# Kernel tuning notes

Hardware: AMD Instinct MI355X
Metric: run time of the kernel (lower is better)

The kernel has to match this reference:

```python
import jax, jax.numpy as jnp
import numpy as np

B, N, L = 1, 2048, 256
DIM_X, DIM_Y, H = 3072, 1536, 24
HD = DIM_X // H  # 128
EPS_MOD = 1e-6   # modulated_rmsnorm eps
EPS_QK = 1e-5    # RMSNorm (q/k norm) eps
NEG = -1e30


def _rms(v, w, eps):
    return v * jax.lax.rsqrt(jnp.mean(v * v, axis=-1, keepdims=True) + eps) * w


def _rope(t, cos, sin):
    # t: (B, N, H, HD); cos/sin: (N, H, HD//2); interleaved even/odd rotation
    te, to = t[..., 0::2], t[..., 1::2]
    c, s = cos[None], sin[None]
    out = jnp.stack([te * c - to * s, te * s + to * c], axis=-1)
    return out.reshape(t.shape)


def _forward(x, y, scale_x, scale_y, rope_cos, rope_sin,
             W_qkv_x, b_qkv_x, W_qkv_y, b_qkv_y,
             w_qnorm_x, w_knorm_x, w_qnorm_y, w_knorm_y,
             W_proj_x, b_proj_x, W_proj_y, b_proj_y, seqlens_y):
    # modulated RMSNorm on x, then fused qkv projection
    xm = x * jax.lax.rsqrt(jnp.mean(x * x, axis=-1, keepdims=True) + EPS_MOD) * (1.0 + scale_x[:, None, :])
    qkv_x = (xm @ W_qkv_x.T + b_qkv_x).reshape(B, N, 3, H, HD)
    q_x, k_x, v_x = qkv_x[:, :, 0], qkv_x[:, :, 1], qkv_x[:, :, 2]
    q_x = _rope(_rms(q_x, w_qnorm_x, EPS_QK), rope_cos, rope_sin)
    k_x = _rope(_rms(k_x, w_knorm_x, EPS_QK), rope_cos, rope_sin)

    ym = y * jax.lax.rsqrt(jnp.mean(y * y, axis=-1, keepdims=True) + EPS_MOD) * (1.0 + scale_y[:, None, :])
    qkv_y = (ym @ W_qkv_y.T + b_qkv_y).reshape(B, L, 3, H, HD)
    q_y, k_y, v_y = qkv_y[:, :, 0], qkv_y[:, :, 1], qkv_y[:, :, 2]
    q_y = _rms(q_y, w_qnorm_y, EPS_QK)
    k_y = _rms(k_y, w_knorm_y, EPS_QK)

    # unify_streams: concat visual + text tokens; flash_attn_varlen over valid
    # tokens == masked dense attention (all x tokens valid, y valid up to seqlens_y)
    q = jnp.concatenate([q_x, q_y], axis=1)  # (B, N+L, H, HD)
    k = jnp.concatenate([k_x, k_y], axis=1)
    v = jnp.concatenate([v_x, v_y], axis=1)
    valid_y = jnp.arange(L)[None, :] < seqlens_y[:, None]          # (B, L)
    valid = jnp.concatenate([jnp.ones((B, N), bool), valid_y], 1)  # (B, N+L)

    scale = HD ** -0.5
    logits = jnp.einsum('bqhd,bkhd->bhqk', q, k) * scale
    logits = jnp.where(valid[:, None, None, :], logits, NEG)
    attn = jax.nn.softmax(logits, axis=-1)
    out = jnp.einsum('bhqk,bkhd->bqhd', attn, v)
    # pad_and_split_xy: invalid positions are zeros (scatter into zero buffer)
    out = jnp.where(valid[:, :, None, None], out, 0.0).reshape(B, N + L, DIM_X)

    x_out = out[:, :N] @ W_proj_x.T + b_proj_x
    y_out = out[:, N:] @ W_proj_y.T + b_proj_y
    return x_out, y_out


def setup_inputs() -> dict:
    key = jax.random.key(0)
    ks = jax.random.split(key, 16)
    f32 = jnp.float32
    theta = jax.random.uniform(ks[4], (N, H, HD // 2), f32, 0.0, 2 * np.pi)
    return {
        'x': jax.random.normal(ks[0], (B, N, DIM_X), f32),
        'y': jax.random.normal(ks[1], (B, L, DIM_Y), f32),
        'scale_x': 0.1 * jax.random.normal(ks[2], (B, DIM_X), f32),
        'scale_y': 0.1 * jax.random.normal(ks[3], (B, DIM_Y), f32),
        'rope_cos': jnp.cos(theta),
        'rope_sin': jnp.sin(theta),
        'seqlens_y': jax.random.randint(ks[5], (B,), 1, L + 1, jnp.int32),
        'W_qkv_x': 0.02 * jax.random.normal(ks[6], (3 * DIM_X, DIM_X), f32),
        'b_qkv_x': jnp.zeros((3 * DIM_X,), f32),
        'W_qkv_y': 0.02 * jax.random.normal(ks[7], (3 * DIM_X, DIM_Y), f32),
        'b_qkv_y': jnp.zeros((3 * DIM_X,), f32),
        'w_qnorm_x': jnp.ones((HD,), f32),
        'w_knorm_x': jnp.ones((HD,), f32),
        'w_qnorm_y': jnp.ones((HD,), f32),
        'w_knorm_y': jnp.ones((HD,), f32),
        'W_proj_x': 0.02 * jax.random.normal(ks[8], (DIM_X, DIM_X), f32),
        'b_proj_x': jnp.zeros((DIM_X,), f32),
        'W_proj_y': 0.02 * jax.random.normal(ks[9], (DIM_Y, DIM_X), f32),
        'b_proj_y': jnp.zeros((DIM_Y,), f32),
    }


def reference(x, y, scale_x, scale_y, rope_cos, rope_sin, seqlens_y,
              W_qkv_x, b_qkv_x, W_qkv_y, b_qkv_y,
              w_qnorm_x, w_knorm_x, w_qnorm_y, w_knorm_y,
              W_proj_x, b_proj_x, W_proj_y, b_proj_y):
    return _forward(x, y, scale_x, scale_y, rope_cos, rope_sin,
                    W_qkv_x, b_qkv_x, W_qkv_y, b_qkv_y,
                    w_qnorm_x, w_knorm_x, w_qnorm_y, w_knorm_y,
                    W_proj_x, b_proj_x, W_proj_y, b_proj_y, seqlens_y)
```

## Files before the change

### kernel.cpp

```cpp
#include <hip/hip_runtime.h>
#include <stdint.h>

#define DEV __device__ __forceinline__

typedef __attribute__((ext_vector_type(8))) short bf16x8;
typedef __attribute__((ext_vector_type(4))) float f32x4;
typedef __attribute__((ext_vector_type(16))) float f32x16;
typedef __attribute__((ext_vector_type(4))) unsigned u32x4;

#define NTOT 2304

DEV unsigned short f2bf(float f) {
  union { float f; unsigned u; } c; c.f = f;
  return (unsigned short)((c.u + 0x7FFFu + ((c.u >> 16) & 1u)) >> 16);
}
DEV unsigned pack2(float lo, float hi) {
  return ((unsigned)f2bf(hi) << 16) | (unsigned)f2bf(lo);
}
DEV unsigned cvtpk(float lo, float hi) {
  unsigned r;
  asm("v_cvt_pk_bf16_f32 %0, %1, %2" : "=v"(r) : "v"(lo), "v"(hi));
  return r;
}
DEV float bf2f(short x) {
  union { unsigned u; float f; } c; c.u = ((unsigned)(unsigned short)x) << 16; return c.f;
}
DEV void gload_lds16(const void* g, void* l) {
  __builtin_amdgcn_global_load_lds(
      (const __attribute__((address_space(1))) unsigned int*)g,
      (__attribute__((address_space(3))) unsigned int*)l, 16, 0, 0);
}
DEV void pl32swap(unsigned& a, unsigned& b) {
  asm volatile("v_permlane32_swap_b32 %0, %1" : "+v"(a), "+v"(b));
}

__global__ __launch_bounds__(256) void k_modnorm(const float* __restrict__ X,
                                                 const float* __restrict__ scale_x,
                                                 short* __restrict__ outx,
                                                 const float* __restrict__ Y,
                                                 const float* __restrict__ scale_y,
                                                 short* __restrict__ outy) {
  int row = blockIdx.x;
  const float* x;
  const float* scale;
  short* o;
  int D;
  if (row < 2048) {
    x = X + (size_t)row * 3072; scale = scale_x; o = outx + (size_t)row * 3072; D = 3072;
  } else {
    row -= 2048;
    x = Y + (size_t)row * 1536; scale = scale_y; o = outy + (size_t)row * 1536; D = 1536;
  }
  float ss = 0.f;
  for (int v = threadIdx.x * 4; v < D; v += 1024) {
    float4 a = *(const float4*)(x + v);
    ss += a.x * a.x + a.y * a.y + a.z * a.z + a.w * a.w;
  }
#pragma unroll
  for (int m = 1; m < 64; m <<= 1) ss += __shfl_xor(ss, m);
  __shared__ float red[4];
  if ((threadIdx.x & 63) == 0) red[threadIdx.x >> 6] = ss;
  __syncthreads();
  float tot = red[0] + red[1] + red[2] + red[3];
  float r = rsqrtf(tot / (float)D + 1e-6f);
  for (int v = threadIdx.x * 4; v < D; v += 1024) {
    float4 a = *(const float4*)(x + v);
    float4 s = *(const float4*)(scale + v);
    uint2 pk;
    pk.x = pack2(a.x * r * (1.f + s.x), a.y * r * (1.f + s.y));
    pk.y = pack2(a.z * r * (1.f + s.z), a.w * r * (1.f + s.w));
    *(uint2*)(o + v) = pk;
  }
}

__global__ __launch_bounds__(256) void k_cvt4(const float* __restrict__ s0, short* __restrict__ d0, int n0,
                                              const float* __restrict__ s1, short* __restrict__ d1, int n1,
                                              const float* __restrict__ s2, short* __restrict__ d2, int n2,
                                              const float* __restrict__ s3, short* __restrict__ d3, int n3) {
  int total = n0 + n1 + n2 + n3;
  int stride = gridDim.x * blockDim.x;
  for (int i = blockIdx.x * blockDim.x + threadIdx.x; i < total; i += stride) {
    const float* s; short* d; int j = i;
    if (j < n0) { s = s0; d = d0; }
    else {
      j -= n0;
      if (j < n1) { s = s1; d = d1; }
      else {
        j -= n1;
        if (j < n2) { s = s2; d = d2; }
        else { j -= n2; s = s3; d = d3; }
      }
    }
    float4 a = *(const float4*)(s + (size_t)j * 4);
    uint2 pk;
    pk.x = pack2(a.x, a.y);
    pk.y = pack2(a.z, a.w);
    *(uint2*)(d + (size_t)j * 4) = pk;
  }
}

__global__ __launch_bounds__(256) void k_gemm(const short* __restrict__ A,
                                              const short* __restrict__ B,
                                              const float* __restrict__ bias,
                                              float* __restrict__ C, int M, int N, int K) {
  __shared__ __align__(16) char As[16384];
  __shared__ __align__(16) char Bs[16384];
  const int tid = threadIdx.x;
  const int brow = blockIdx.y * 128, bcol = blockIdx.x * 128;
  const int w = tid >> 6, l = tid & 63;
  const int wr = (w >> 1) * 64, wc = (w & 1) * 64;
  const int lr = l & 15, lg = l >> 4;
  f32x4 acc[4][4];
#pragma unroll
  for (int m = 0; m < 4; ++m)
#pragma unroll
    for (int n = 0; n < 4; ++n) acc[m][n] = (f32x4){0.f, 0.f, 0.f, 0.f};
  for (int k0 = 0; k0 < K; k0 += 64) {
#pragma unroll
    for (int it = 0; it < 4; ++it) {
      int o = it * 4096 + tid * 16;
      int row = o >> 7;
      int gs = ((o >> 4) & 7) ^ (row & 7);
      gload_lds16(A + (size_t)(brow + row) * K + k0 + gs * 8, As + o);
      gload_lds16(B + (size_t)(bcol + row) * K + k0 + gs * 8, Bs + o);
    }
    __syncthreads();
#pragma unroll
    for (int ks = 0; ks < 2; ++ks) {
      bf16x8 af[4], bfr[4];
#pragma unroll
      for (int m = 0; m < 4; ++m) {
        int ra = wr + m * 16 + lr;
        af[m] = *(const bf16x8*)(As + ra * 128 + (((ks * 4 + lg) ^ (ra & 7)) << 4));
        int rb = wc + m * 16 + lr;
        bfr[m] = *(const bf16x8*)(Bs + rb * 128 + (((ks * 4 + lg) ^ (rb & 7)) << 4));
      }
#pragma unroll
      for (int m = 0; m < 4; ++m)
#pragma unroll
        for (int n = 0; n < 4; ++n)
          acc[m][n] = __builtin_amdgcn_mfma_f32_16x16x32_bf16(bfr[n], af[m], acc[m][n], 0, 0, 0);
    }
    __syncthreads();
  }
#pragma unroll
  for (int m = 0; m < 4; ++m) {
    int row = brow + wr + m * 16 + lr;
#pragma unroll
    for (int n = 0; n < 4; ++n) {
      int col = bcol + wc + n * 16 + lg * 4;
      float4 bv = *(const float4*)(bias + col);
      float4 o;
      o.x = acc[m][n][0] + bv.x;
      o.y = acc[m][n][1] + bv.y;
      o.z = acc[m][n][2] + bv.z;
      o.w = acc[m][n][3] + bv.w;
      *(float4*)(C + (size_t)row * N + col) = o;
    }
  }
}

__global__ __launch_bounds__(256) void k_gemm_qkv(const short* __restrict__ A,
                                                  const short* __restrict__ B,
                                                  const float* __restrict__ bias,
                                                  short* __restrict__ Qb, short* __restrict__ Kb,
                                                  short* __restrict__ Vb,
                                                  int K, int col0, int base_n) {
  __shared__ __align__(16) char As[16384];
  __shared__ __align__(16) char Bs[16384];
  const int tid = threadIdx.x;
  const int brow = blockIdx.y * 128, bcol = blockIdx.x * 128;
  const int w = tid >> 6, l = tid & 63;
  const int wr = (w >> 1) * 64, wc = (w & 1) * 64;
  const int lr = l & 15, lg = l >> 4;
  f32x4 acc[4][4];
#pragma unroll
  for (int m = 0; m < 4; ++m)
#pragma unroll
    for (int n = 0; n < 4; ++n) acc[m][n] = (f32x4){0.f, 0.f, 0.f, 0.f};
  for (int k0 = 0; k0 < K; k0 += 64) {
#pragma unroll
    for (int it = 0; it < 4; ++it) {
      int o = it * 4096 + tid * 16;
      int row = o >> 7;
      int gs = ((o >> 4) & 7) ^ (row & 7);
      gload_lds16(A + (size_t)(brow + row) * K + k0 + gs * 8, As + o);
      gload_lds16(B + (size_t)(bcol + row) * K + k0 + gs * 8, Bs + o);
    }
    __syncthreads();
#pragma unroll
    for (int ks = 0; ks < 2; ++ks) {
      bf16x8 af[4], bfr[4];
#pragma unroll
      for (int m = 0; m < 4; ++m) {
        int ra = wr + m * 16 + lr;
        af[m] = *(const bf16x8*)(As + ra * 128 + (((ks * 4 + lg) ^ (ra & 7)) << 4));
        int rb = wc + m * 16 + lr;
        bfr[m] = *(const bf16x8*)(Bs + rb * 128 + (((ks * 4 + lg) ^ (rb & 7)) << 4));
      }
#pragma unroll
      for (int m = 0; m < 4; ++m)
#pragma unroll
        for (int n = 0; n < 4; ++n)
          acc[m][n] = __builtin_amdgcn_mfma_f32_16x16x32_bf16(bfr[n], af[m], acc[m][n], 0, 0, 0);
    }
    __syncthreads();
  }
#pragma unroll
  for (int m = 0; m < 4; ++m) {
    int row = brow + wr + m * 16 + lr;
#pragma unroll
    for (int n = 0; n < 4; ++n) {
      int colg = col0 + bcol + wc + n * 16 + lg * 4;
      float4 bv = *(const float4*)(bias + colg);
      int ty = colg / 3072;
      int rem = colg - ty * 3072;
      int h = rem >> 7, d = rem & 127;
      short* dst = (ty == 0) ? Qb : ((ty == 1) ? Kb : Vb);
      uint2 pk;
      pk.x = pack2(acc[m][n][0] + bv.x, acc[m][n][1] + bv.y);
      pk.y = pack2(acc[m][n][2] + bv.z, acc[m][n][3] + bv.w);
      *(uint2*)(dst + ((size_t)(h * NTOT + base_n + row)) * 128 + d) = pk;
    }
  }
}

__global__ __launch_bounds__(512, 2) void k_g256(const short* __restrict__ A,
                                                 const short* __restrict__ B,
                                                 const float* __restrict__ bias,
                                                 short* __restrict__ Qb, short* __restrict__ Kb,
                                                 short* __restrict__ Vb, int K) {
  __shared__ __align__(16) char lds[131072];
  const int tid = threadIdx.x;
  const int w = tid >> 6, l = tid & 63;
  const int lr = l & 15, lg = l >> 4;
  const int wm = w >> 2, wn = w & 3;
  const int brow = blockIdx.y * 256, bcol = blockIdx.x * 256;
  const int nt = K >> 6;

  auto issue = [&](int g) {
    if (g >= 4 * nt) return;
    int tt = g >> 2, hh = g & 3;
    char* base = lds + (tt & 1) * 65536;
    if (hh < 2) {
#pragma unroll
      for (int j = 0; j < 2; ++j) {
        int ch = hh * 1024 + j * 512 + tid;
        int row = ch >> 3, c = ch & 7;
        gload_lds16(A + (size_t)(brow + row) * K + tt * 64 + ((c ^ (row & 7)) << 3),
                    base + ch * 16);
      }
    } else {
      int hb = hh - 2;
#pragma unroll
      for (int j = 0; j < 2; ++j) {
        int ch = hb * 1024 + j * 512 + tid;
        int row = ch >> 3, c = ch & 7;
        gload_lds16(B + (size_t)(bcol + row) * K + tt * 64 + ((c ^ (row & 7)) << 3),
                    base + 32768 + ch * 16);
      }
    }
  };

  f32x4 acc[8][4];
#pragma unroll
  for (int m = 0; m < 8; ++m)
#pragma unroll
    for (int n = 0; n < 4; ++n) acc[m][n] = (f32x4){0.f, 0.f, 0.f, 0.f};

#pragma unroll
  for (int g = 0; g < 6; ++g) issue(g);
  asm volatile("s_waitcnt vmcnt(4)" ::: "memory");
  __builtin_amdgcn_s_barrier();

  bf16x8 af[8][2], bf[4][2];
  for (int t = 0; t < nt; ++t) {
    const char* bb = lds + (t & 1) * 65536;
    const int g0 = 4 * t + 6;
#pragma unroll
    for (int m = 0; m < 4; ++m) {
      int r = wm * 128 + m * 16 + lr;
#pragma unroll
      for (int ks = 0; ks < 2; ++ks)
        af[m][ks] = *(const bf16x8*)(bb + r * 128 + (((ks * 4 + lg) ^ (r & 7)) << 4));
    }
#pragma unroll
    for (int n = 0; n < 2; ++n) {
      int r = wn * 64 + n * 16 + lr;
#pragma unroll
      for (int ks = 0; ks < 2; ++ks)
        bf[n][ks] = *(const bf16x8*)(bb + 32768 + r * 128 + (((ks * 4 + lg) ^ (r & 7)) << 4));
    }
    issue(g0);
    __builtin_amdgcn_s_barrier();
    __builtin_amdgcn_s_setprio(1);
#pragma unroll
    for (int m = 0; m < 4; ++m)
#pragma unroll
      for (int n = 0; n < 2; ++n)
#pragma unroll
        for (int ks = 0; ks < 2; ++ks)
          acc[m][n] = __builtin_amdgcn_mfma_f32_16x16x32_bf16(bf[n][ks], af[m][ks], acc[m][n], 0, 0, 0);
    __builtin_amdgcn_s_setprio(0);
    __builtin_amdgcn_sched_barrier(0);
    __builtin_amdgcn_s_barrier();
#pragma unroll
    for (int n = 2; n < 4; ++n) {
      int r = wn * 64 + n * 16 + lr;
#pragma unroll
      for (int ks = 0; ks < 2; ++ks)
        bf[n][ks] = *(const bf16x8*)(bb + 32768 + r * 128 + (((ks * 4 + lg) ^ (r & 7)) << 4));
    }
    issue(g0 + 1);
    __builtin_amdgcn_s_barrier();
    __builtin_amdgcn_s_setprio(1);
#pragma unroll
    for (int m = 0; m < 4; ++m)
#pragma unroll
      for (int n = 2; n < 4; ++n)
#pragma unroll
        for (int ks = 0; ks < 2; ++ks)
          acc[m][n] = __builtin_amdgcn_mfma_f32_16x16x32_bf16(bf[n][ks], af[m][ks], acc[m][n], 0, 0, 0);
    __builtin_amdgcn_s_setprio(0);
    __builtin_amdgcn_sched_barrier(0);
    __builtin_amdgcn_s_barrier();
#pragma unroll
    for (int m = 4; m < 8; ++m) {
      int r = wm * 128 + m * 16 + lr;
#pragma unroll
      for (int ks = 0; ks < 2; ++ks)
        af[m][ks] = *(const bf16x8*)(bb + r * 128 + (((ks * 4 + lg) ^ (r & 7)) << 4));
    }
    __builtin_amdgcn_s_barrier();
    __builtin_amdgcn_s_setprio(1);
#pragma unroll
    for (int m = 4; m < 8; ++m)
#pragma unroll
      for (int n = 2; n < 4; ++n)
#pragma unroll
        for (int ks = 0; ks < 2; ++ks)
          acc[m][n] = __builtin_amdgcn_mfma_f32_16x16x32_bf16(bf[n][ks], af[m][ks], acc[m][n], 0, 0, 0);
    __builtin_amdgcn_s_setprio(0);
    __builtin_amdgcn_sched_barrier(0);
    __builtin_amdgcn_s_barrier();
    issue(g0 + 2);
    issue(g0 + 3);
    __builtin_amdgcn_s_barrier();
    __builtin_amdgcn_s_setprio(1);
#pragma unroll
    for (int m = 4; m < 8; ++m)
#pragma unroll
      for (int n = 0; n < 2; ++n)
#pragma unroll
        for (int ks = 0; ks < 2; ++ks)
          acc[m][n] = __builtin_amdgcn_mfma_f32_16x16x32_bf16(bf[n][ks], af[m][ks], acc[m][n], 0, 0, 0);
    __builtin_amdgcn_s_setprio(0);
    __builtin_amdgcn_sched_barrier(0);
    if (t + 2 < nt)
      asm volatile("s_waitcnt vmcnt(4)" ::: "memory");
    else
      asm volatile("s_waitcnt vmcnt(0)" ::: "memory");
    __builtin_amdgcn_s_barrier();
  }

#pragma unroll
  for (int m = 0; m < 8; ++m) {
    int row = brow + wm * 128 + m * 16 + lr;
#pragma unroll
    for (int n = 0; n < 4; ++n) {
      int colg = bcol + wn * 64 + n * 16 + lg * 4;
      float4 bv = *(const float4*)(bias + colg);
      int ty = colg / 3072;
      int rem = colg - ty * 3072;
      int h = rem >> 7, d = rem & 127;
      short* dst = (ty == 0) ? Qb : ((ty == 1) ? Kb : Vb);
      uint2 pk;
      pk.x = pack2(acc[m][n][0] + bv.x, acc[m][n][1] + bv.y);
      pk.y = pack2(acc[m][n][2] + bv.z, acc[m][n][3] + bv.w);
      *(uint2*)(dst + ((size_t)(h * NTOT + row)) * 128 + d) = pk;
    }
  }
}

__global__ __launch_bounds__(256) void k_post2(short* __restrict__ Qb, short* __restrict__ Kb,
                                               const float* __restrict__ wqx,
                                               const float* __restrict__ wkx,
                                               const float* __restrict__ wqy,
                                               const float* __restrict__ wky,
                                               const float* __restrict__ cosb,
                                               const float* __restrict__ sinb) {
  int idx = blockIdx.x * 4 + (threadIdx.x >> 6);
  int l = threadIdx.x & 63;
  const float* wq;
  const float* wk;
  int n, h, base_n;
  bool rope;
  if (idx < 49152) {
    n = idx / 24; h = idx - n * 24; base_n = 0; wq = wqx; wk = wkx; rope = true;
  } else {
    int j = idx - 49152;
    n = j / 24; h = j - n * 24; base_n = 2048; wq = wqy; wk = wky; rope = false;
  }
  size_t off = ((size_t)h * NTOT + base_n + n) * 128 + 2 * l;
  unsigned qu = *(unsigned*)(Qb + off);
  unsigned ku = *(unsigned*)(Kb + off);
  float qx = bf2f((short)(qu & 0xFFFF)), qy = bf2f((short)(qu >> 16));
  float kx = bf2f((short)(ku & 0xFFFF)), ky = bf2f((short)(ku >> 16));
  float sq = qx * qx + qy * qy;
  float sk = kx * kx + ky * ky;
#pragma unroll
  for (int m = 1; m < 64; m <<= 1) {
    sq += __shfl_xor(sq, m);
    sk += __shfl_xor(sk, m);
  }
  float rq = rsqrtf(sq * (1.f / 128.f) + 1e-5f);
  float rk = rsqrtf(sk * (1.f / 128.f) + 1e-5f);
  float2 wqv = *(const float2*)(wq + 2 * l);
  float2 wkv = *(const float2*)(wk + 2 * l);
  qx = qx * rq * wqv.x; qy = qy * rq * wqv.y;
  kx = kx * rk * wkv.x; ky = ky * rk * wkv.y;
  if (rope) {
    float c = cosb[(size_t)idx * 64 + l];
    float s = sinb[(size_t)idx * 64 + l];
    float t;
    t = qx * c - qy * s; qy = qx * s + qy * c; qx = t;
    t = kx * c - ky * s; ky = kx * s + ky * c; kx = t;
  }
  *(unsigned*)(Qb + off) = pack2(qx, qy);
  *(unsigned*)(Kb + off) = pack2(kx, ky);
}

__global__ __launch_bounds__(256) void k_transpose(const short* __restrict__ V,
                                                   short* __restrict__ VT) {
  __shared__ __align__(16) short tile[64][72];
  int h = blockIdx.z;
  int n0 = blockIdx.x * 64, d0 = blockIdx.y * 64;
  int tid = threadIdx.x;
#pragma unroll
  for (int it = 0; it < 2; ++it) {
    int nl = it * 32 + (tid >> 3);
    int dl = (tid & 7) * 8;
    *(bf16x8*)&tile[nl][dl] = *(const bf16x8*)(V + ((size_t)h * NTOT + n0 + nl) * 128 + d0 + dl);
  }
  __syncthreads();
#pragma unroll
  for (int it = 0; it < 2; ++it) {
    int dl = it * 32 + (tid >> 3);
    int nl = (tid & 7) * 8;
    bf16x8 o;
#pragma unroll
    for (int j = 0; j < 8; ++j) o[j] = tile[nl + j][dl];
    *(bf16x8*)(VT + ((size_t)h * 128 + d0 + dl) * NTOT + n0 + nl) = o;
  }
}

__global__ __launch_bounds__(256, 2) void k_attn32(const short* __restrict__ Qb,
                                                   const short* __restrict__ Kb,
                                                   const short* __restrict__ VT,
                                                   const int* __restrict__ seqlens,
                                                   short* __restrict__ Ob) {
  __shared__ __align__(16) char lds[65536];
  const int tid = threadIdx.x;
  const int w = tid >> 6, l = tid & 63;
  const int l31 = l & 31, hi = l >> 5;
  int orig = blockIdx.x;
  int wg = (orig & 7) * 54 + (orig >> 3);
  int h = wg / 18, qb = wg - h * 18;
  const int q0 = qb * 128;
  const size_t hK = (size_t)h * NTOT * 128;
  const size_t hV = (size_t)h * 128 * NTOT;
  const int kvlim = 2048 + seqlens[0];
  const int nt = (kvlim + 63) >> 6;

  const float qs = 0.08838834764831845f * 1.44269504088896340f;
  bf16x8 qf[8];
  {
    const short* qrow = Qb + hK + (size_t)(q0 + w * 32 + l31) * 128;
#pragma unroll
    for (int s = 0; s < 8; ++s) {
      bf16x8 r = *(const bf16x8*)(qrow + s * 16 + hi * 8);
      union { unsigned u[4]; bf16x8 b; } cv;
#pragma unroll
      for (int d = 0; d < 4; ++d)
        cv.u[d] = cvtpk(bf2f(r[2 * d]) * qs, bf2f(r[2 * d + 1]) * qs);
      qf[s] = cv.b;
    }
  }

  f32x16 acc[4];
#pragma unroll
  for (int d0 = 0; d0 < 4; ++d0)
#pragma unroll
    for (int r = 0; r < 16; ++r) acc[d0][r] = 0.f;
  float mrun = -1e30f, lsum = 0.f;

  auto stage = [&](int t, int buf) {
    int kv0 = t * 64;
    char* bK = lds + buf * 32768;
    char* bV = bK + 16384;
#pragma unroll
    for (int it = 0; it < 4; ++it) {
      int o = it * 4096 + tid * 16;
      int rk = o >> 8, sk = (o >> 4) & 15;
      int mk = (rk & 7) ^ ((rk >> 3) & 3);
      gload_lds16(Kb + hK + (size_t)(kv0 + rk) * 128 + ((sk ^ mk) << 3), bK + o);
      int rv = o >> 7, sv = (o >> 4) & 7;
      gload_lds16(VT + hV + (size_t)rv * NTOT + kv0 + ((sv ^ (rv & 7)) << 3), bV + o);
    }
  };

  stage(0, 0);
  asm volatile("s_waitcnt vmcnt(0)");
  __syncthreads();

  int cur = 0;
  for (int t = 0; t < nt; ++t) {
    if (t + 1 < nt) stage(t + 1, cur ^ 1);
    const char* bK = lds + cur * 32768;
    const char* bV = bK + 16384;
    f32x16 st[2];
#pragma unroll
    for (int hf = 0; hf < 2; ++hf)
#pragma unroll
      for (int r = 0; r < 16; ++r) st[hf][r] = 0.f;
#pragma unroll
    for (int hf = 0; hf < 2; ++hf) {
      int row = hf * 32 + l31;
      int mk = (row & 7) ^ ((row >> 3) & 3);
#pragma unroll
      for (int s = 0; s < 8; ++s) {
        bf16x8 kf = *(const bf16x8*)(bK + row * 256 + (((s * 2 + hi) ^ mk) << 4));
        st[hf] = __builtin_amdgcn_mfma_f32_32x32x16_bf16(kf, qf[s], st[hf], 0, 0, 0);
      }
    }
    if (t == nt - 1) {
      int kv0 = t * 64;
#pragma unroll
      for (int hf = 0; hf < 2; ++hf)
#pragma unroll
        for (int r = 0; r < 16; ++r) {
          int kv = kv0 + hf * 32 + (r & 3) + 8 * (r >> 2) + 4 * hi;
          if (kv >= kvlim) st[hf][r] = -1e30f;
        }
    }
    float tm[8];
#pragma unroll
    for (int i = 0; i < 8; ++i)
      tm[i] = fmaxf(fmaxf(st[0][2 * i], st[0][2 * i + 1]),
                    fmaxf(st[1][2 * i], st[1][2 * i + 1]));
    float tmax = fmaxf(fmaxf(fmaxf(tm[0], tm[1]), fmaxf(tm[2], tm[3])),
                       fmaxf(fmaxf(tm[4], tm[5]), fmaxf(tm[6], tm[7])));
    tmax = fmaxf(tmax, __shfl_xor(tmax, 32));
    if (!__all(tmax - mrun <= 11.54f)) {
      float mnew = fmaxf(mrun, tmax);
      float corr = __builtin_amdgcn_exp2f(mrun - mnew);
      mrun = mnew;
      lsum *= corr;
#pragma unroll
      for (int d0 = 0; d0 < 4; ++d0)
#pragma unroll
        for (int r = 0; r < 16; ++r) acc[d0][r] *= corr;
    }
    float ts = 0.f;
#pragma unroll
    for (int hf = 0; hf < 2; ++hf)
#pragma unroll
      for (int r = 0; r < 16; ++r) {
        float p = __builtin_amdgcn_exp2f(st[hf][r] - mrun);
        st[hf][r] = p;
        ts += p;
      }
    ts += __shfl_xor(ts, 32);
    lsum += ts;
    bf16x8 pa[4];
#pragma unroll
    for (int hf = 0; hf < 2; ++hf) {
      unsigned x0 = cvtpk(st[hf][0], st[hf][1]);
      unsigned y0 = cvtpk(st[hf][4], st[hf][5]);
      pl32swap(x0, y0);
      unsigned z0 = cvtpk(st[hf][2], st[hf][3]);
      unsigned w0 = cvtpk(st[hf][6], st[hf][7]);
      pl32swap(z0, w0);
      { union { u32x4 u; bf16x8 b; } cv; cv.u = (u32x4){x0, z0, y0, w0}; pa[hf * 2 + 0] = cv.b; }
      unsigned x1 = cvtpk(st[hf][8], st[hf][9]);
      unsigned y1 = cvtpk(st[hf][12], st[hf][13]);
      pl32swap(x1, y1);
      unsigned z1 = cvtpk(st[hf][10], st[hf][11]);
      unsigned w1 = cvtpk(st[hf][14], st[hf][15]);
      pl32swap(z1, w1);
      { union { u32x4 u; bf16x8 b; } cv; cv.u = (u32x4){x1, z1, y1, w1}; pa[hf * 2 + 1] = cv.b; }
    }
#pragma unroll
    for (int d0 = 0; d0 < 4; ++d0) {
      int row = d0 * 32 + l31;
      int rx = row & 7;
#pragma unroll
      for (int s4 = 0; s4 < 4; ++s4) {
        bf16x8 va = *(const bf16x8*)(bV + row * 128 + (((s4 * 2 + hi) ^ rx) << 4));
        acc[d0] = __builtin_amdgcn_mfma_f32_32x32x16_bf16(va, pa[s4], acc[d0], 0, 0, 0);
      }
    }
    asm volatile("s_waitcnt vmcnt(0)");
    __syncthreads();
    cur ^= 1;
  }

  {
    char* ob = lds;
    int qloc = w * 32 + l31;
    int qg = q0 + qloc;
    float inv = (qg < kvlim) ? 1.f / lsum : 0.f;
#pragma unroll
    for (int d0 = 0; d0 < 4; ++d0)
#pragma unroll
      for (int g = 0; g < 4; ++g) {
        int dbase = d0 * 32 + 8 * g + 4 * hi;
        uint2 pk;
        pk.x = cvtpk(acc[d0][4 * g + 0] * inv, acc[d0][4 * g + 1] * inv);
        pk.y = cvtpk(acc[d0][4 * g + 2] * inv, acc[d0][4 * g + 3] * inv);
        int off = dbase * 2;
        int off2 = ((((off >> 4) ^ (qloc & 7)) << 4) | (off & 8));
        *(uint2*)(ob + qloc * 256 + off2) = pk;
      }
    __syncthreads();
    int qr = tid >> 1, dh = tid & 1;
#pragma unroll
    for (int j = 0; j < 8; ++j) {
      int slot = dh * 8 + j;
      bf16x8 v = *(const bf16x8*)(ob + qr * 256 + ((slot ^ (qr & 7)) << 4));
      *(bf16x8*)(Ob + (size_t)(q0 + qr) * 3072 + h * 128 + slot * 8) = v;
    }
  }
}

extern "C" void kernel_launch(void* const* d_in, const int* in_sizes, int n_in,
                              void* d_out, int out_size, void* d_ws, size_t ws_size,
                              hipStream_t stream) {
  const float* x       = (const float*)d_in[0];
  const float* y       = (const float*)d_in[1];
  const float* scale_x = (const float*)d_in[2];
  const float* scale_y = (const float*)d_in[3];
  const float* ropec   = (const float*)d_in[4];
  const float* ropes   = (const float*)d_in[5];
  const int*   seqlens = (const int*)d_in[6];
  const float* Wqx     = (const float*)d_in[7];
  const float* bqx     = (const float*)d_in[8];
  const float* Wqy     = (const float*)d_in[9];
  const float* bqy     = (const float*)d_in[10];
  const float* wqnx    = (const float*)d_in[11];
  const float* wknx    = (const float*)d_in[12];
  const float* wqny    = (const float*)d_in[13];
  const float* wkny    = (const float*)d_in[14];
  const float* Wpx     = (const float*)d_in[15];
  const float* bpx     = (const float*)d_in[16];
  const float* Wpy     = (const float*)d_in[17];
  const float* bpy     = (const float*)d_in[18];
  float* out = (float*)d_out;
  (void)in_sizes; (void)n_in; (void)out_size; (void)ws_size;

  char* ws = (char*)d_ws;
  size_t off = 0;
  auto alloc = [&](size_t bytes) {
    char* p = ws + off;
    off += (bytes + 255) & ~(size_t)255;
    return p;
  };
  short* xm   = (short*)alloc((size_t)2048 * 3072 * 2);
  short* ym   = (short*)alloc((size_t)256 * 1536 * 2);
  short* wqxb = (short*)alloc((size_t)9216 * 3072 * 2);
  short* wqyb = (short*)alloc((size_t)9216 * 1536 * 2);
  short* wpxb = (short*)alloc((size_t)3072 * 3072 * 2);
  short* wpyb = (short*)alloc((size_t)1536 * 3072 * 2);
  short* Qb   = (short*)alloc((size_t)24 * NTOT * 128 * 2);
  short* Kb   = (short*)alloc((size_t)24 * NTOT * 128 * 2);
  short* Vb   = (short*)alloc((size_t)24 * NTOT * 128 * 2);
  short* VTb  = (short*)alloc((size_t)24 * NTOT * 128 * 2);
  short* AO   = (short*)alloc((size_t)NTOT * 3072 * 2);

  hipLaunchKernelGGL(k_modnorm, dim3(2304), dim3(256), 0, stream, x, scale_x, xm, y, scale_y, ym);
  hipLaunchKernelGGL(k_cvt4, dim3(2048), dim3(256), 0, stream,
                     Wqx, wqxb, 9216 * 3072 / 4, Wqy, wqyb, 9216 * 1536 / 4,
                     Wpx, wpxb, 3072 * 3072 / 4, Wpy, wpyb, 1536 * 3072 / 4);
  hipLaunchKernelGGL(k_g256, dim3(32, 8), dim3(512), 0, stream, xm, wqxb, bqx, Qb, Kb, Vb, 3072);
  hipLaunchKernelGGL(k_gemm_qkv, dim3(8, 16), dim3(256), 0, stream, xm,
                     wqxb + (size_t)8192 * 3072, bqx, Qb, Kb, Vb, 3072, 8192, 0);
  hipLaunchKernelGGL(k_gemm_qkv, dim3(72, 2), dim3(256), 0, stream, ym, wqyb, bqy,
                     Qb, Kb, Vb, 1536, 0, 2048);
  hipLaunchKernelGGL(k_post2, dim3(13824), dim3(256), 0, stream, Qb, Kb,
                     wqnx, wknx, wqny, wkny, ropec, ropes);
  hipLaunchKernelGGL(k_transpose, dim3(36, 2, 24), dim3(256), 0, stream, Vb, VTb);
  hipLaunchKernelGGL(k_attn32, dim3(432), dim3(256), 0, stream, Qb, Kb, VTb, seqlens, AO);
  hipLaunchKernelGGL(k_gemm, dim3(24, 16), dim3(256), 0, stream, AO, wpxb, bpx, out, 2048, 3072, 3072);
  hipLaunchKernelGGL(k_gemm, dim3(12, 2), dim3(256), 0, stream, AO + (size_t)2048 * 3072, wpyb, bpy,
                     out + (size_t)2048 * 3072, 256, 1536, 3072);
}
```

Measured before the change: 504.3 us.

## Restructure 256x256 GEMM main loop with register double-buffered fragments and prefetch

```diff
diff --git a/kernel.cpp b/kernel.cpp
--- a/kernel.cpp
+++ b/kernel.cpp
@@ -225,6 +225,51 @@
   }
 }
 
+#define LDFRAG(BUF, R, KS) \
+  (*(const bf16x8*)((BUF) + (R) * 128 + ((((KS) * 4 + lg) ^ ((R) & 7)) << 4)))
+
+#define RDAP(DST, M0, BUF) do { \
+  _Pragma("unroll") for (int i_ = 0; i_ < 2; ++i_) { \
+    int r_ = wm * 128 + ((M0) + i_) * 16 + lr; \
+    DST[i_][0] = LDFRAG(BUF, r_, 0); \
+    DST[i_][1] = LDFRAG(BUF, r_, 1); } } while (0)
+
+#define RDBF(DST, BUF) do { \
+  _Pragma("unroll") for (int n_ = 0; n_ < 4; ++n_) { \
+    int r_ = wn * 64 + n_ * 16 + lr; \
+    DST[n_][0] = LDFRAG((BUF) + 32768, r_, 0); \
+    DST[n_][1] = LDFRAG((BUF) + 32768, r_, 1); } } while (0)
+
+#define MFMA4(MP, AP, BF) do { \
+  __builtin_amdgcn_s_setprio(1); \
+  _Pragma("unroll") for (int i_ = 0; i_ < 2; ++i_) \
+    _Pragma("unroll") for (int n_ = 0; n_ < 4; ++n_) { \
+      acc[2*(MP)+i_][n_] = __builtin_amdgcn_mfma_f32_16x16x32_bf16(BF[n_][0], AP[i_][0], acc[2*(MP)+i_][n_], 0, 0, 0); \
+      acc[2*(MP)+i_][n_] = __builtin_amdgcn_mfma_f32_16x16x32_bf16(BF[n_][1], AP[i_][1], acc[2*(MP)+i_][n_], 0, 0, 0); } \
+  __builtin_amdgcn_s_setprio(0); } while (0)
+
+#define TILE(T, BB, NB, BFC, BFN) do { \
+  __builtin_amdgcn_s_barrier(); \
+  RDAP(apB, 2, BB); \
+  __builtin_amdgcn_sched_barrier(0); \
+  MFMA4(0, apA, BFC); \
+  __builtin_amdgcn_s_barrier(); \
+  RDAP(apA, 4, BB); \
+  __builtin_amdgcn_sched_barrier(0); \
+  MFMA4(1, apB, BFC); \
+  __builtin_amdgcn_s_barrier(); \
+  RDAP(apB, 6, BB); \
+  __builtin_amdgcn_sched_barrier(0); \
+  MFMA4(2, apA, BFC); \
+  asm volatile("s_waitcnt vmcnt(0)" ::: "memory"); \
+  __builtin_amdgcn_s_barrier(); \
+  if ((T) + 1 < nt) { RDBF(BFN, NB); RDAP(apA, 0, NB); } \
+  issue(4 * ((T) + 2));     issue(4 * ((T) + 2) + 1); \
+  issue(4 * ((T) + 2) + 2); issue(4 * ((T) + 2) + 3); \
+  __builtin_amdgcn_sched_barrier(0); \
+  MFMA4(3, apB, BFC); \
+} while (0)
+
 __global__ __launch_bounds__(512, 2) void k_g256(const short* __restrict__ A,
                                                  const short* __restrict__ B,
                                                  const float* __restrict__ bias,
@@ -268,99 +313,21 @@
 #pragma unroll
     for (int n = 0; n < 4; ++n) acc[m][n] = (f32x4){0.f, 0.f, 0.f, 0.f};
 
-#pragma unroll
-  for (int g = 0; g < 6; ++g) issue(g);
-  asm volatile("s_waitcnt vmcnt(4)" ::: "memory");
+  bf16x8 bfA[4][2], bfB[4][2];
+  bf16x8 apA[2][2], apB[2][2];
+  const char* b0 = lds;
+  const char* b1 = lds + 65536;
+
+#pragma unroll
+  for (int g = 0; g < 8; ++g) issue(g);
+  asm volatile("s_waitcnt vmcnt(8)" ::: "memory");
   __builtin_amdgcn_s_barrier();
-
-  bf16x8 af[8][2], bf[4][2];
-  for (int t = 0; t < nt; ++t) {
-    const char* bb = lds + (t & 1) * 65536;
-    const int g0 = 4 * t + 6;
-#pragma unroll
-    for (int m = 0; m < 4; ++m) {
-      int r = wm * 128 + m * 16 + lr;
-#pragma unroll
-      for (int ks = 0; ks < 2; ++ks)
-        af[m][ks] = *(const bf16x8*)(bb + r * 128 + (((ks * 4 + lg) ^ (r & 7)) << 4));
-    }
-#pragma unroll
-    for (int n = 0; n < 2; ++n) {
-      int r = wn * 64 + n * 16 + lr;
-#pragma unroll
-      for (int ks = 0; ks < 2; ++ks)
-        bf[n][ks] = *(const bf16x8*)(bb + 32768 + r * 128 + (((ks * 4 + lg) ^ (r & 7)) << 4));
-    }
-    issue(g0);
-    __builtin_amdgcn_s_barrier();
-    __builtin_amdgcn_s_setprio(1);
-#pragma unroll
-    for (int m = 0; m < 4; ++m)
-#pragma unroll
-      for (int n = 0; n < 2; ++n)
-#pragma unroll
-        for (int ks = 0; ks < 2; ++ks)
-          acc[m][n] = __builtin_amdgcn_mfma_f32_16x16x32_bf16(bf[n][ks], af[m][ks], acc[m][n], 0, 0, 0);
-    __builtin_amdgcn_s_setprio(0);
-    __builtin_amdgcn_sched_barrier(0);
-    __builtin_amdgcn_s_barrier();
-#pragma unroll
-    for (int n = 2; n < 4; ++n) {
-      int r = wn * 64 + n * 16 + lr;
-#pragma unroll
-      for (int ks = 0; ks < 2; ++ks)
-        bf[n][ks] = *(const bf16x8*)(bb + 32768 + r * 128 + (((ks * 4 + lg) ^ (r & 7)) << 4));
-    }
-    issue(g0 + 1);
-    __builtin_amdgcn_s_barrier();
-    __builtin_amdgcn_s_setprio(1);
-#pragma unroll
-    for (int m = 0; m < 4; ++m)
-#pragma unroll
-      for (int n = 2; n < 4; ++n)
-#pragma unroll
-        for (int ks = 0; ks < 2; ++ks)
-          acc[m][n] = __builtin_amdgcn_mfma_f32_16x16x32_bf16(bf[n][ks], af[m][ks], acc[m][n], 0, 0, 0);
-    __builtin_amdgcn_s_setprio(0);
-    __builtin_amdgcn_sched_barrier(0);
-    __builtin_amdgcn_s_barrier();
-#pragma unroll
-    for (int m = 4; m < 8; ++m) {
-      int r = wm * 128 + m * 16 + lr;
-#pragma unroll
-      for (int ks = 0; ks < 2; ++ks)
-        af[m][ks] = *(const bf16x8*)(bb + r * 128 + (((ks * 4 + lg) ^ (r & 7)) << 4));
-    }
-    __builtin_amdgcn_s_barrier();
-    __builtin_amdgcn_s_setprio(1);
-#pragma unroll
-    for (int m = 4; m < 8; ++m)
-#pragma unroll
-      for (int n = 2; n < 4; ++n)
-#pragma unroll
-        for (int ks = 0; ks < 2; ++ks)
-          acc[m][n] = __builtin_amdgcn_mfma_f32_16x16x32_bf16(bf[n][ks], af[m][ks], acc[m][n], 0, 0, 0);
-    __builtin_amdgcn_s_setprio(0);
-    __builtin_amdgcn_sched_barrier(0);
-    __builtin_amdgcn_s_barrier();
-    issue(g0 + 2);
-    issue(g0 + 3);
-    __builtin_amdgcn_s_barrier();
-    __builtin_amdgcn_s_setprio(1);
-#pragma unroll
-    for (int m = 4; m < 8; ++m)
-#pragma unroll
-      for (int n = 0; n < 2; ++n)
-#pragma unroll
-        for (int ks = 0; ks < 2; ++ks)
-          acc[m][n] = __builtin_amdgcn_mfma_f32_16x16x32_bf16(bf[n][ks], af[m][ks], acc[m][n], 0, 0, 0);
-    __builtin_amdgcn_s_setprio(0);
-    __builtin_amdgcn_sched_barrier(0);
-    if (t + 2 < nt)
-      asm volatile("s_waitcnt vmcnt(4)" ::: "memory");
-    else
-      asm volatile("s_waitcnt vmcnt(0)" ::: "memory");
-    __builtin_amdgcn_s_barrier();
+  RDBF(bfA, b0);
+  RDAP(apA, 0, b0);
+
+  for (int t = 0; t < nt; t += 2) {
+    TILE(t, b0, b1, bfA, bfB);
+    TILE(t + 1, b1, b0, bfB, bfA);
   }
 
 #pragma unroll
```

Result: slower. 568.0 us (+12.6%).
